# Kernel tuning notes

Hardware: AMD Instinct MI355X
Metric: run time of the kernel (lower is better)

## Reference

```python
import jax, jax.numpy as jnp
import numpy as np

B, N, D, NE, NB = 512, 128, 64, 6, 4

def setup_inputs() -> dict:
    key = jax.random.key(0)
    ks = jax.random.split(key, 24)
    inp = {}
    inp['atom_types'] = jax.random.randint(ks[0], (B, N), 0, NE, dtype=jnp.int32)
    inp['positions'] = jax.random.normal(ks[1], (B, N, 3), dtype=jnp.float32)
    inp['bonds'] = jax.random.randint(ks[2], (B, N, N), 0, 5, dtype=jnp.int32)
    s = 0.05
    inp['emb'] = jax.random.normal(ks[3], (NE, D), dtype=jnp.float32)
    inp['ae_w'] = jax.random.normal(ks[4], (D,), dtype=jnp.float32) * s
    inp['ae_b'] = jax.random.normal(ks[5], (), dtype=jnp.float32) * s
    inp['ent_w'] = jax.random.normal(ks[6], (D,), dtype=jnp.float32) * s
    inp['ent_b'] = jax.random.normal(ks[7], (), dtype=jnp.float32) * s
    inp['bW'] = jax.random.normal(ks[8], (NB, D, D), dtype=jnp.float32) * s
    inp['bb'] = jax.random.normal(ks[9], (NB,), dtype=jnp.float32) * s
    H = N * D
    inp['sW1'] = jax.random.normal(ks[10], (H, 256), dtype=jnp.float32) * s
    inp['sb1'] = jnp.zeros((256,), jnp.float32)
    inp['sW2'] = jax.random.normal(ks[11], (256, 128), dtype=jnp.float32) * s
    inp['sb2'] = jnp.zeros((128,), jnp.float32)
    inp['sW3'] = jax.random.normal(ks[12], (128, 1), dtype=jnp.float32) * s
    inp['sb3'] = jnp.zeros((1,), jnp.float32)
    inp['dW1'] = jax.random.normal(ks[13], (H, 256), dtype=jnp.float32) * s
    inp['db1'] = jnp.zeros((256,), jnp.float32)
    inp['dW2'] = jax.random.normal(ks[14], (256, 128), dtype=jnp.float32) * s
    inp['db2'] = jnp.zeros((128,), jnp.float32)
    inp['dW3'] = jax.random.normal(ks[15], (128, 1), dtype=jnp.float32) * s
    inp['db3'] = jnp.zeros((1,), jnp.float32)
    return inp

def _mlp(x, W1, b1, W2, b2, W3, b3):
    h = jax.nn.relu(x @ W1 + b1)
    h = jax.nn.relu(h @ W2 + b2)
    return jax.nn.sigmoid((h @ W3 + b3)[..., 0])

def reference(atom_types, positions, bonds, emb, ae_w, ae_b, ent_w, ent_b, bW, bb,
              sW1, sb1, sW2, sb2, sW3, sb3, dW1, db1, dW2, db2, dW3, db3):
    x = emb[atom_types]                                    # [B,N,D]
    atomic_e = jnp.einsum('bnd,d->bn', x, ae_w) + ae_b     # atomic_energy linear
    atomic_s = jnp.einsum('bnd,d->bn', x, ent_w) + ent_b   # atomic_entropy linear

    # Pairwise bilinear bond energies: e[b,i,j,k] = x_i^T W_k x_j + bb_k
    t = jnp.einsum('bid,kde->bike', x, bW)                 # [B,N,K,D]
    e_all = jnp.einsum('bike,bje->bijk', t, x) + bb        # [B,N,N,K]
    bt = bonds - 1                                         # bond type index
    upper = jnp.triu(jnp.ones((N, N), dtype=bool), k=1)    # i < j
    bond_mask = upper[None] & (bonds > 0) & (bt < NB)
    e_sel = jnp.take_along_axis(e_all, jnp.clip(bt, 0, NB - 1)[..., None].astype(jnp.int32), axis=-1)[..., 0]
    bond_e = jnp.sum(jnp.where(bond_mask, e_sel, 0.0), axis=(1, 2))

    # Lennard-Jones style vdW over all i<j pairs
    diff = positions[:, :, None, :] - positions[:, None, :, :]   # [B,N,N,3]
    dist = jnp.sqrt(jnp.sum(diff * diff, axis=-1))
    vmask = upper[None] & (dist > 0)
    inv = 1.0 / jnp.where(dist > 0, dist, 1.0)
    vdw = 4.0 * (inv ** 12 - inv ** 6) * 0.1
    vdw_e = jnp.sum(jnp.where(vmask, vdw, 0.0), axis=(1, 2))

    energy = atomic_e.sum(axis=1) + bond_e + vdw_e

    # entropy: unbiased variance over atoms, summed over xyz
    pos_var = jnp.var(positions, axis=1, ddof=1).sum(axis=-1)
    entropy = atomic_s.sum(axis=1) + jnp.log(1.0 + pos_var)

    mol = x.reshape(x.shape[0], -1)                        # [B, N*D]
    stability = _mlp(mol, sW1, sb1, sW2, sb2, sW3, sb3)
    druglikeness = _mlp(mol, dW1, db1, dW2, db2, dW3, db3)
    return (energy, entropy, stability, druglikeness, x)
```

## Files before the change

### kernel.cpp

```cpp
#include <hip/hip_runtime.h>
#include <math.h>

#define BB_ 512
#define NN_ 128
#define DD_ 64
#define NE_ 6
#define NB_ 4

#define WS_PAIRE 0
#define WS_E1    160
#define U16BASE_ 1024
#define TDOFF_   (768 * 256)
#define W2OFF_   (1536 * 256)

typedef unsigned short u16x8 __attribute__((ext_vector_type(8)));

__device__ __forceinline__ ushort f2b(float f) {
  unsigned u = __float_as_uint(f);
  u += 0x7FFFu + ((u >> 16) & 1u);
  return (ushort)(u >> 16);
}
__device__ __forceinline__ float b2f(ushort h) {
  return __uint_as_float(((unsigned)h) << 16);
}

__device__ __forceinline__ float block_reduce256(float v, volatile float* red4,
                                                 int tid) {
#pragma unroll
  for (int off = 32; off > 0; off >>= 1) v += __shfl_down(v, off);
  __syncthreads();
  if ((tid & 63) == 0) red4[tid >> 6] = v;
  __syncthreads();
  return red4[0] + red4[1] + red4[2] + red4[3];
}

__global__ __launch_bounds__(256, 4) void k_a(
    const float* __restrict__ emb, const float* __restrict__ ae_w,
    const float* __restrict__ ae_b, const float* __restrict__ ent_w,
    const float* __restrict__ ent_b, const float* __restrict__ bW,
    const float* __restrict__ sW1, const float* __restrict__ dW1,
    const float* __restrict__ sW2, const float* __restrict__ dW2,
    const int* __restrict__ atom_types, const float* __restrict__ pos,
    float* __restrict__ ws, float* __restrict__ out) {
  int id = blockIdx.x;
  int tid = threadIdx.x;
  ushort* U = (ushort*)(ws + U16BASE_);
  __shared__ float smem[1160];
  volatile float* red4 = smem + 1152;

  if (id < 1536) {
    int m = id / 3;
    int c = id - m * 3;
    if (c == 0) {
      int n = m >> 2;
      int which = (m >> 1) & 1;
      int ohalf = m & 1;
      const float* W1 = which ? dW1 : sW1;
      ushort* T = U + (which ? TDOFF_ : 0);
      float* e_s = smem;
      float* part = smem + 384;
      for (int i = tid; i < NE_ * DD_; i += 256) e_s[i] = emb[i];
      __syncthreads();
      int o_local = tid & 127;
      int dhalf = tid >> 7;
      int o = ohalf * 128 + o_local;
      float acc[NE_] = {0.f, 0.f, 0.f, 0.f, 0.f, 0.f};
      const float* Wp = W1 + ((size_t)(n * DD_ + dhalf * 32)) * 256 + o;
#pragma unroll 8
      for (int d = 0; d < 32; ++d) {
        float w = Wp[(size_t)d * 256];
#pragma unroll
        for (int t = 0; t < NE_; ++t)
          acc[t] += e_s[t * DD_ + dhalf * 32 + d] * w;
      }
      if (dhalf == 1) {
#pragma unroll
        for (int t = 0; t < NE_; ++t) part[t * 128 + o_local] = acc[t];
      }
      __syncthreads();
      if (dhalf == 0) {
#pragma unroll
        for (int t = 0; t < NE_; ++t)
          T[(n * NE_ + t) * 256 + o] = f2b(acc[t] + part[t * 128 + o_local]);
      }
    } else if (c == 1) {
      float* e_s = smem;
      unsigned char* tyb = (unsigned char*)(smem + 384);
      for (int i = tid; i < NE_ * DD_; i += 256) e_s[i] = emb[i];
      if (tid < 32) {
        int4 t4 = ((const int4*)(atom_types + (size_t)m * NN_))[tid];
        uchar4 u4;
        u4.x = (unsigned char)t4.x;
        u4.y = (unsigned char)t4.y;
        u4.z = (unsigned char)t4.z;
        u4.w = (unsigned char)t4.w;
        ((uchar4*)tyb)[tid] = u4;
      }
      __syncthreads();
      float4* out4 = (float4*)(out + 2048 + (size_t)m * (NN_ * DD_));
#pragma unroll
      for (int u = 0; u < 8; ++u) {
        int li = tid + (u << 8);
        int n = li >> 4;
        int d0 = (li & 15) << 2;
        out4[li] = *(const float4*)&e_s[tyb[n] * DD_ + d0];
      }
    } else {
      float4* p4 = (float4*)smem;
      float* aev = smem + 520;
      float* entv = smem + 528;
      float* redm = smem + 544;
      if (tid < 128) {
        const float* pm = pos + (size_t)m * NN_ * 3 + 3 * tid;
        p4[tid] = make_float4(pm[0], pm[1], pm[2], 0.f);
      } else if (tid < 224) {
        int v = (tid - 128) >> 3;
        int l8 = tid & 7;
        int t = v - (v >= 6 ? 6 : 0);
        const float* wv = (v >= 6) ? ent_w : ae_w;
        const float* er = emb + t * DD_ + l8 * 8;
        const float* wr = wv + l8 * 8;
        float s = 0.f;
#pragma unroll
        for (int u = 0; u < 8; ++u) s += er[u] * wr[u];
#pragma unroll
        for (int off = 4; off > 0; off >>= 1) s += __shfl_down(s, off, 8);
        if (l8 == 0) {
          if (v < 6)
            aev[v] = s + ae_b[0];
          else
            entv[v - 6] = s + ent_b[0];
        }
      }
      __syncthreads();

      int i = tid >> 1;
      int half = tid & 1;
      float4 pi = p4[i];
      float vp = 0.f;
#pragma unroll 8
      for (int u = 0; u < 64; ++u) {
        int j = (half << 6) + u;
        float4 pj = p4[j];
        float dx = pi.x - pj.x;
        float dy = pi.y - pj.y;
        float dz = pi.z - pj.z;
        float d2 = dx * dx + dy * dy + dz * dz;
        if (j > i && d2 > 0.f) {
          float rc = __builtin_amdgcn_rcpf(d2);
          float r6 = rc * rc * rc;
          vp += 0.4f * (r6 * r6 - r6);
        }
      }

      float x = 0.f, y = 0.f, z = 0.f, sq = 0.f, ae = 0.f, en = 0.f;
      if (tid < 128) {
        float4 p = p4[tid];
        x = p.x;
        y = p.y;
        z = p.z;
        sq = x * x + y * y + z * z;
        int t = atom_types[(size_t)m * NN_ + tid];
        ae = aev[t];
        en = entv[t];
      }
      float vals[7] = {vp, x, y, z, sq, ae, en};
#pragma unroll
      for (int v = 0; v < 7; ++v) {
#pragma unroll
        for (int off = 32; off > 0; off >>= 1)
          vals[v] += __shfl_down(vals[v], off);
      }
      int wv2 = tid >> 6, ln = tid & 63;
      if (ln == 0) {
#pragma unroll
        for (int v = 0; v < 7; ++v) redm[wv2 * 8 + v] = vals[v];
      }
      __syncthreads();
      if (tid == 0) {
        float S[7];
#pragma unroll
        for (int v = 0; v < 7; ++v)
          S[v] = redm[v] + redm[8 + v] + redm[16 + v] + redm[24 + v];
        float var = (S[4] - (S[1] * S[1] + S[2] * S[2] + S[3] * S[3]) *
                                (1.f / NN_)) *
                    (1.f / (NN_ - 1));
        ws[WS_E1 + m] = S[0] + S[5];
        out[BB_ + m] = S[6] + logf(1.f + var);
      }
    }
  } else if (id < 1680) {
    int e = id - 1536;
    int k = e / 36;
    int rem = e - k * 36;
    int ti = rem / 6, tj = rem - (rem / 6) * 6;
    int d = tid & 63;
    int qd = tid >> 6;
    const float* Wrow = bW + ((size_t)k * DD_ + d) * DD_ + qd * 16;
    const float* xj = emb + tj * DD_ + qd * 16;
    float a = 0.f;
#pragma unroll
    for (int u = 0; u < 16; ++u) a += Wrow[u] * xj[u];
    float c = emb[ti * DD_ + d] * a;
    c = block_reduce256(c, red4, tid);
    if (tid == 0) ws[WS_PAIRE + e] = c;
  } else {
    int base = (id - 1680) * 4096 + tid;
#pragma unroll
    for (int u = 0; u < 16; ++u) {
      int e = base + u * 256;
      int head = e >> 15;
      int idx = e & 32767;
      const float* src = head ? dW2 : sW2;
      U[W2OFF_ + e] = f2b(src[idx]);
    }
  }
}

__global__ __launch_bounds__(256, 4) void k_b(
    const int* __restrict__ atom_types, const int* __restrict__ bonds,
    const float* __restrict__ bb, const float* __restrict__ sb1,
    const float* __restrict__ sb2, const float* __restrict__ sW3,
    const float* __restrict__ sb3, const float* __restrict__ db1,
    const float* __restrict__ db2, const float* __restrict__ dW3,
    const float* __restrict__ db3, const float* __restrict__ ws,
    float* __restrict__ out) {
  int id = blockIdx.x;
  int tid = threadIdx.x;
  const ushort* U = (const ushort*)(ws + U16BASE_);
  __shared__ float smem[2632];
  volatile float* red4 = smem + 2624;

  if ((id & 1) == 0) {
    int m = id >> 1;
    float* pE = smem;
    float* bbv = smem + 144;
    unsigned char* tyb = (unsigned char*)(smem + 160);

    if (tid < 32) {
      int4 t4 = ((const int4*)(atom_types + (size_t)m * NN_))[tid];
      uchar4 u4;
      u4.x = (unsigned char)t4.x;
      u4.y = (unsigned char)t4.y;
      u4.z = (unsigned char)t4.z;
      u4.w = (unsigned char)t4.w;
      ((uchar4*)tyb)[tid] = u4;
    }
    if (tid >= 64 && tid < 208) pE[tid - 64] = ws[WS_PAIRE + tid - 64];
    if (tid >= 224 && tid < 228) bbv[tid - 224] = bb[tid - 224];
    __syncthreads();

    const int4* b4 = (const int4*)(bonds + (size_t)m * NN_ * NN_);
    float bp = 0.f;
#pragma unroll 4
    for (int it = 0; it < 16; ++it) {
      int li = tid + (it << 8);
      int i = li >> 5;
      int c = li & 31;
      if (c * 4 + 3 > i) {
        int4 v = b4[li];
        int j0 = c << 2;
        int ti6 = tyb[i] * 6;
        if (j0 + 0 > i && v.x > 0)
          bp += pE[(v.x - 1) * 36 + ti6 + tyb[j0 + 0]] + bbv[v.x - 1];
        if (j0 + 1 > i && v.y > 0)
          bp += pE[(v.y - 1) * 36 + ti6 + tyb[j0 + 1]] + bbv[v.y - 1];
        if (j0 + 2 > i && v.z > 0)
          bp += pE[(v.z - 1) * 36 + ti6 + tyb[j0 + 2]] + bbv[v.z - 1];
        if (j0 + 3 > i && v.w > 0)
          bp += pE[(v.w - 1) * 36 + ti6 + tyb[j0 + 3]] + bbv[v.w - 1];
      }
    }
    float e = block_reduce256(bp, red4, tid);
    if (tid == 0) out[m] = e + ws[WS_E1 + m];
  } else {
    int mlpid = id >> 1;
    int which = mlpid & 1;
    int mbase = (mlpid >> 1) * 2;
    float* part = smem;
    float* scr = smem;
    float* h2 = smem + 512;
    float* h1 = smem + 2048;
    unsigned char* tyb = (unsigned char*)(smem + 2560);

    tyb[tid] = (unsigned char)atom_types[(size_t)mbase * NN_ + tid];
    __syncthreads();

    {
      int mi = tid >> 7;
      int q = (tid >> 5) & 3;
      int ot = tid & 31;
      const ushort* Tb = U + (which ? TDOFF_ : 0) + ot * 8;
      const unsigned char* ty = tyb + mi * NN_;
      float a[8] = {0.f, 0.f, 0.f, 0.f, 0.f, 0.f, 0.f, 0.f};
      int nb = q * 32;
      for (int n0 = 0; n0 < 32; n0 += 8) {
        u16x8 v[8];
#pragma unroll
        for (int u = 0; u < 8; ++u) {
          int n = nb + n0 + u;
          v[u] = *(const u16x8*)(Tb + ((n * 6 + (int)ty[n]) << 8));
        }
#pragma unroll
        for (int u = 0; u < 8; ++u) {
#pragma unroll
          for (int j = 0; j < 8; ++j) a[j] += b2f(v[u][j]);
        }
      }
      float* pp = part + mi * 1024 + q * 256 + ot * 8;
#pragma unroll
      for (int j = 0; j < 8; ++j) pp[j] = a[j];
    }
    __syncthreads();
    {
#pragma unroll
      for (int li = tid; li < 512; li += 256) {
        int mm = li >> 8;
        int o = li & 255;
        float s = part[mm * 1024 + o] + part[mm * 1024 + 256 + o] +
                  part[mm * 1024 + 512 + o] + part[mm * 1024 + 768 + o];
        h1[li] = fmaxf(s + (which ? db1 : sb1)[o], 0.f);
      }
    }
    __syncthreads();

    {
      int k = tid & 127;
      int kh = tid >> 7;
      const ushort* Wp = U + W2OFF_ + which * 32768 + kh * 16384 + k;
      float acc[2] = {0.f, 0.f};
      for (int o0 = 0; o0 < 128; o0 += 16) {
        float wf[16];
#pragma unroll
        for (int u = 0; u < 16; ++u) wf[u] = b2f(Wp[(o0 + u) << 7]);
#pragma unroll
        for (int mm = 0; mm < 2; ++mm) {
          const float* hp = h1 + mm * 256 + kh * 128 + o0;
          float s = 0.f;
#pragma unroll
          for (int u = 0; u < 16; ++u) s += hp[u] * wf[u];
          acc[mm] += s;
        }
      }
      scr[kh * 256 + 0 * 128 + k] = acc[0];
      scr[kh * 256 + 1 * 128 + k] = acc[1];
    }
    __syncthreads();
    if (tid < 128) {
      float b2v = (which ? db2 : sb2)[tid];
#pragma unroll
      for (int mm = 0; mm < 2; ++mm)
        h2[mm * 128 + tid] =
            fmaxf(b2v + scr[mm * 128 + tid] + scr[256 + mm * 128 + tid], 0.f);
    }
    __syncthreads();

    {
      int mm = tid >> 5;
      int ln = tid & 31;
      if (mm < 2) {
        const float* W3 = which ? dW3 : sW3;
        float s = 0.f;
#pragma unroll
        for (int u = 0; u < 4; ++u) {
          int kk = ln + (u << 5);
          s += h2[mm * 128 + kk] * W3[kk];
        }
#pragma unroll
        for (int off = 16; off > 0; off >>= 1) s += __shfl_down(s, off, 32);
        if (ln == 0) {
          float b3 = (which ? db3 : sb3)[0];
          out[(2 + which) * BB_ + mbase + mm] = 1.f / (1.f + __expf(-(s + b3)));
        }
      }
    }
  }
}

extern "C" void kernel_launch(void* const* d_in, const int* in_sizes, int n_in,
                              void* d_out, int out_size, void* d_ws,
                              size_t ws_size, hipStream_t stream) {
  const int* atom_types = (const int*)d_in[0];
  const float* positions = (const float*)d_in[1];
  const int* bonds = (const int*)d_in[2];
  const float* emb = (const float*)d_in[3];
  const float* ae_w = (const float*)d_in[4];
  const float* ae_b = (const float*)d_in[5];
  const float* ent_w = (const float*)d_in[6];
  const float* ent_b = (const float*)d_in[7];
  const float* bW = (const float*)d_in[8];
  const float* bb = (const float*)d_in[9];
  const float* sW1 = (const float*)d_in[10];
  const float* sb1 = (const float*)d_in[11];
  const float* sW2 = (const float*)d_in[12];
  const float* sb2 = (const float*)d_in[13];
  const float* sW3 = (const float*)d_in[14];
  const float* sb3 = (const float*)d_in[15];
  const float* dW1 = (const float*)d_in[16];
  const float* db1 = (const float*)d_in[17];
  const float* dW2 = (const float*)d_in[18];
  const float* db2 = (const float*)d_in[19];
  const float* dW3 = (const float*)d_in[20];
  const float* db3 = (const float*)d_in[21];
  float* out = (float*)d_out;
  float* ws = (float*)d_ws;

  hipLaunchKernelGGL(k_a, dim3(1696), dim3(256), 0, stream, emb, ae_w, ae_b,
                     ent_w, ent_b, bW, sW1, dW1, sW2, dW2, atom_types,
                     positions, ws, out);
  hipLaunchKernelGGL(k_b, dim3(1024), dim3(256), 0, stream, atom_types, bonds,
                     bb, sb1, sb2, sW3, sb3, db1, db2, dW3, db3, ws, out);
}
```

Baseline: 28.08 us.

## Move independent per-molecule work from first kernel into second kernel

The vdW/entropy reduction and the embedding gather into the output do not depend on the precomputed tables, so they move from k_a into k_b. k_b now runs four block roles per molecule (2048 blocks), while k_a shrinks to the table-building work plus one block that zeroes the energy output. Energy is combined with atomicAdd from the bond and vdW blocks. The aim is a shorter dependency-bound first kernel and better-filled second launch, at the cost of atomics and a larger, more heterogeneous k_b.

```diff
diff --git a/kernel.cpp b/kernel.cpp
--- a/kernel.cpp
+++ b/kernel.cpp
@@ -8,7 +8,6 @@
 #define NB_ 4
 
 #define WS_PAIRE 0
-#define WS_E1    160
 #define U16BASE_ 1024
 #define TDOFF_   (768 * 256)
 #define W2OFF_   (1536 * 256)
@@ -35,162 +34,47 @@
 }
 
 __global__ __launch_bounds__(256, 4) void k_a(
-    const float* __restrict__ emb, const float* __restrict__ ae_w,
-    const float* __restrict__ ae_b, const float* __restrict__ ent_w,
-    const float* __restrict__ ent_b, const float* __restrict__ bW,
+    const float* __restrict__ emb, const float* __restrict__ bW,
     const float* __restrict__ sW1, const float* __restrict__ dW1,
     const float* __restrict__ sW2, const float* __restrict__ dW2,
-    const int* __restrict__ atom_types, const float* __restrict__ pos,
     float* __restrict__ ws, float* __restrict__ out) {
-  int id = blockIdx.x;
+  int blk = blockIdx.x;
   int tid = threadIdx.x;
   ushort* U = (ushort*)(ws + U16BASE_);
-  __shared__ float smem[1160];
-  volatile float* red4 = smem + 1152;
-
-  if (id < 1536) {
-    int m = id / 3;
-    int c = id - m * 3;
-    if (c == 0) {
-      int n = m >> 2;
-      int which = (m >> 1) & 1;
-      int ohalf = m & 1;
-      const float* W1 = which ? dW1 : sW1;
-      ushort* T = U + (which ? TDOFF_ : 0);
-      float* e_s = smem;
-      float* part = smem + 384;
-      for (int i = tid; i < NE_ * DD_; i += 256) e_s[i] = emb[i];
-      __syncthreads();
-      int o_local = tid & 127;
-      int dhalf = tid >> 7;
-      int o = ohalf * 128 + o_local;
-      float acc[NE_] = {0.f, 0.f, 0.f, 0.f, 0.f, 0.f};
-      const float* Wp = W1 + ((size_t)(n * DD_ + dhalf * 32)) * 256 + o;
+
+  if (blk < 512) {
+    int n = blk >> 2;
+    int which = (blk >> 1) & 1;
+    int ohalf = blk & 1;
+    const float* W1 = which ? dW1 : sW1;
+    ushort* T = U + (which ? TDOFF_ : 0);
+    __shared__ float e_s[NE_ * DD_];
+    __shared__ float part[NE_][128];
+    for (int i = tid; i < NE_ * DD_; i += 256) e_s[i] = emb[i];
+    __syncthreads();
+    int o_local = tid & 127;
+    int dhalf = tid >> 7;
+    int o = ohalf * 128 + o_local;
+    float acc[NE_] = {0.f, 0.f, 0.f, 0.f, 0.f, 0.f};
+    const float* Wp = W1 + ((size_t)(n * DD_ + dhalf * 32)) * 256 + o;
 #pragma unroll 8
-      for (int d = 0; d < 32; ++d) {
-        float w = Wp[(size_t)d * 256];
-#pragma unroll
-        for (int t = 0; t < NE_; ++t)
-          acc[t] += e_s[t * DD_ + dhalf * 32 + d] * w;
-      }
-      if (dhalf == 1) {
-#pragma unroll
-        for (int t = 0; t < NE_; ++t) part[t * 128 + o_local] = acc[t];
-      }
-      __syncthreads();
-      if (dhalf == 0) {
-#pragma unroll
-        for (int t = 0; t < NE_; ++t)
-          T[(n * NE_ + t) * 256 + o] = f2b(acc[t] + part[t * 128 + o_local]);
-      }
-    } else if (c == 1) {
-      float* e_s = smem;
-      unsigned char* tyb = (unsigned char*)(smem + 384);
-      for (int i = tid; i < NE_ * DD_; i += 256) e_s[i] = emb[i];
-      if (tid < 32) {
-        int4 t4 = ((const int4*)(atom_types + (size_t)m * NN_))[tid];
-        uchar4 u4;
-        u4.x = (unsigned char)t4.x;
-        u4.y = (unsigned char)t4.y;
-        u4.z = (unsigned char)t4.z;
-        u4.w = (unsigned char)t4.w;
-        ((uchar4*)tyb)[tid] = u4;
-      }
-      __syncthreads();
-      float4* out4 = (float4*)(out + 2048 + (size_t)m * (NN_ * DD_));
-#pragma unroll
-      for (int u = 0; u < 8; ++u) {
-        int li = tid + (u << 8);
-        int n = li >> 4;
-        int d0 = (li & 15) << 2;
-        out4[li] = *(const float4*)&e_s[tyb[n] * DD_ + d0];
-      }
-    } else {
-      float4* p4 = (float4*)smem;
-      float* aev = smem + 520;
-      float* entv = smem + 528;
-      float* redm = smem + 544;
-      if (tid < 128) {
-        const float* pm = pos + (size_t)m * NN_ * 3 + 3 * tid;
-        p4[tid] = make_float4(pm[0], pm[1], pm[2], 0.f);
-      } else if (tid < 224) {
-        int v = (tid - 128) >> 3;
-        int l8 = tid & 7;
-        int t = v - (v >= 6 ? 6 : 0);
-        const float* wv = (v >= 6) ? ent_w : ae_w;
-        const float* er = emb + t * DD_ + l8 * 8;
-        const float* wr = wv + l8 * 8;
-        float s = 0.f;
-#pragma unroll
-        for (int u = 0; u < 8; ++u) s += er[u] * wr[u];
-#pragma unroll
-        for (int off = 4; off > 0; off >>= 1) s += __shfl_down(s, off, 8);
-        if (l8 == 0) {
-          if (v < 6)
-            aev[v] = s + ae_b[0];
-          else
-            entv[v - 6] = s + ent_b[0];
-        }
-      }
-      __syncthreads();
-
-      int i = tid >> 1;
-      int half = tid & 1;
-      float4 pi = p4[i];
-      float vp = 0.f;
-#pragma unroll 8
-      for (int u = 0; u < 64; ++u) {
-        int j = (half << 6) + u;
-        float4 pj = p4[j];
-        float dx = pi.x - pj.x;
-        float dy = pi.y - pj.y;
-        float dz = pi.z - pj.z;
-        float d2 = dx * dx + dy * dy + dz * dz;
-        if (j > i && d2 > 0.f) {
-          float rc = __builtin_amdgcn_rcpf(d2);
-          float r6 = rc * rc * rc;
-          vp += 0.4f * (r6 * r6 - r6);
-        }
-      }
-
-      float x = 0.f, y = 0.f, z = 0.f, sq = 0.f, ae = 0.f, en = 0.f;
-      if (tid < 128) {
-        float4 p = p4[tid];
-        x = p.x;
-        y = p.y;
-        z = p.z;
-        sq = x * x + y * y + z * z;
-        int t = atom_types[(size_t)m * NN_ + tid];
-        ae = aev[t];
-        en = entv[t];
-      }
-      float vals[7] = {vp, x, y, z, sq, ae, en};
-#pragma unroll
-      for (int v = 0; v < 7; ++v) {
-#pragma unroll
-        for (int off = 32; off > 0; off >>= 1)
-          vals[v] += __shfl_down(vals[v], off);
-      }
-      int wv2 = tid >> 6, ln = tid & 63;
-      if (ln == 0) {
-#pragma unroll
-        for (int v = 0; v < 7; ++v) redm[wv2 * 8 + v] = vals[v];
-      }
-      __syncthreads();
-      if (tid == 0) {
-        float S[7];
-#pragma unroll
-        for (int v = 0; v < 7; ++v)
-          S[v] = redm[v] + redm[8 + v] + redm[16 + v] + redm[24 + v];
-        float var = (S[4] - (S[1] * S[1] + S[2] * S[2] + S[3] * S[3]) *
-                                (1.f / NN_)) *
-                    (1.f / (NN_ - 1));
-        ws[WS_E1 + m] = S[0] + S[5];
-        out[BB_ + m] = S[6] + logf(1.f + var);
-      }
-    }
-  } else if (id < 1680) {
-    int e = id - 1536;
+    for (int d = 0; d < 32; ++d) {
+      float w = Wp[(size_t)d * 256];
+#pragma unroll
+      for (int t = 0; t < NE_; ++t) acc[t] += e_s[t * DD_ + dhalf * 32 + d] * w;
+    }
+    if (dhalf == 1) {
+#pragma unroll
+      for (int t = 0; t < NE_; ++t) part[t][o_local] = acc[t];
+    }
+    __syncthreads();
+    if (dhalf == 0) {
+#pragma unroll
+      for (int t = 0; t < NE_; ++t)
+        T[(n * NE_ + t) * 256 + o] = f2b(acc[t] + part[t][o_local]);
+    }
+  } else if (blk < 656) {
+    int e = blk - 512;
     int k = e / 36;
     int rem = e - k * 36;
     int ti = rem / 6, tj = rem - (rem / 6) * 6;
@@ -202,10 +86,11 @@
 #pragma unroll
     for (int u = 0; u < 16; ++u) a += Wrow[u] * xj[u];
     float c = emb[ti * DD_ + d] * a;
+    __shared__ float red4[4];
     c = block_reduce256(c, red4, tid);
     if (tid == 0) ws[WS_PAIRE + e] = c;
-  } else {
-    int base = (id - 1680) * 4096 + tid;
+  } else if (blk < 672) {
+    int base = (blk - 656) * 4096 + tid;
 #pragma unroll
     for (int u = 0; u < 16; ++u) {
       int e = base + u * 256;
@@ -214,11 +99,16 @@
       const float* src = head ? dW2 : sW2;
       U[W2OFF_ + e] = f2b(src[idx]);
     }
+  } else {
+    ((float2*)out)[tid] = make_float2(0.f, 0.f);
   }
 }
 
 __global__ __launch_bounds__(256, 4) void k_b(
-    const int* __restrict__ atom_types, const int* __restrict__ bonds,
+    const int* __restrict__ atom_types, const float* __restrict__ pos,
+    const int* __restrict__ bonds, const float* __restrict__ emb,
+    const float* __restrict__ ae_w, const float* __restrict__ ae_b,
+    const float* __restrict__ ent_w, const float* __restrict__ ent_b,
     const float* __restrict__ bb, const float* __restrict__ sb1,
     const float* __restrict__ sb2, const float* __restrict__ sW3,
     const float* __restrict__ sb3, const float* __restrict__ db1,
@@ -226,13 +116,14 @@
     const float* __restrict__ db3, const float* __restrict__ ws,
     float* __restrict__ out) {
   int id = blockIdx.x;
+  int c = id & 3;
+  int m = id >> 2;
   int tid = threadIdx.x;
   const ushort* U = (const ushort*)(ws + U16BASE_);
-  __shared__ float smem[2632];
-  volatile float* red4 = smem + 2624;
-
-  if ((id & 1) == 0) {
-    int m = id >> 1;
+  __shared__ float smem[2640];
+  volatile float* red4 = smem + 2632;
+
+  if (c == 0) {
     float* pE = smem;
     float* bbv = smem + 144;
     unsigned char* tyb = (unsigned char*)(smem + 160);
@@ -256,10 +147,10 @@
     for (int it = 0; it < 16; ++it) {
       int li = tid + (it << 8);
       int i = li >> 5;
-      int c = li & 31;
-      if (c * 4 + 3 > i) {
+      int cc = li & 31;
+      if (cc * 4 + 3 > i) {
         int4 v = b4[li];
-        int j0 = c << 2;
+        int j0 = cc << 2;
         int ti6 = tyb[i] * 6;
         if (j0 + 0 > i && v.x > 0)
           bp += pE[(v.x - 1) * 36 + ti6 + tyb[j0 + 0]] + bbv[v.x - 1];
@@ -272,9 +163,114 @@
       }
     }
     float e = block_reduce256(bp, red4, tid);
-    if (tid == 0) out[m] = e + ws[WS_E1 + m];
+    if (tid == 0) atomicAdd(&out[m], e);
+  } else if (c == 1) {
+    float4* p4 = (float4*)smem;
+    float* aev = smem + 520;
+    float* entv = smem + 528;
+    float* redm = smem + 544;
+    if (tid < 128) {
+      const float* pm = pos + (size_t)m * NN_ * 3 + 3 * tid;
+      p4[tid] = make_float4(pm[0], pm[1], pm[2], 0.f);
+    } else if (tid < 224) {
+      int v = (tid - 128) >> 3;
+      int l8 = tid & 7;
+      int t = v - (v >= 6 ? 6 : 0);
+      const float* wv = (v >= 6) ? ent_w : ae_w;
+      const float* er = emb + t * DD_ + l8 * 8;
+      const float* wr = wv + l8 * 8;
+      float s = 0.f;
+#pragma unroll
+      for (int u = 0; u < 8; ++u) s += er[u] * wr[u];
+#pragma unroll
+      for (int off = 4; off > 0; off >>= 1) s += __shfl_down(s, off, 8);
+      if (l8 == 0) {
+        if (v < 6)
+          aev[v] = s + ae_b[0];
+        else
+          entv[v - 6] = s + ent_b[0];
+      }
+    }
+    __syncthreads();
+
+    int i = tid >> 1;
+    int half = tid & 1;
+    float4 pi = p4[i];
+    float vp = 0.f;
+#pragma unroll 8
+    for (int u = 0; u < 64; ++u) {
+      int j = (half << 6) + u;
+      float4 pj = p4[j];
+      float dx = pi.x - pj.x;
+      float dy = pi.y - pj.y;
+      float dz = pi.z - pj.z;
+      float d2 = dx * dx + dy * dy + dz * dz;
+      if (j > i && d2 > 0.f) {
+        float rc = __builtin_amdgcn_rcpf(d2);
+        float r6 = rc * rc * rc;
+        vp += 0.4f * (r6 * r6 - r6);
+      }
+    }
+
+    float x = 0.f, y = 0.f, z = 0.f, sq = 0.f, ae = 0.f, en = 0.f;
+    if (tid < 128) {
+      float4 p = p4[tid];
+      x = p.x;
+      y = p.y;
+      z = p.z;
+      sq = x * x + y * y + z * z;
+      int t = atom_types[(size_t)m * NN_ + tid];
+      ae = aev[t];
+      en = entv[t];
+    }
+    float vals[7] = {vp, x, y, z, sq, ae, en};
+#pragma unroll
+    for (int v = 0; v < 7; ++v) {
+#pragma unroll
+      for (int off = 32; off > 0; off >>= 1)
+        vals[v] += __shfl_down(vals[v], off);
+    }
+    int wv2 = tid >> 6, ln = tid & 63;
+    if (ln == 0) {
+#pragma unroll
+      for (int v = 0; v < 7; ++v) redm[wv2 * 8 + v] = vals[v];
+    }
+    __syncthreads();
+    if (tid == 0) {
+      float S[7];
+#pragma unroll
+      for (int v = 0; v < 7; ++v)
+        S[v] = redm[v] + redm[8 + v] + redm[16 + v] + redm[24 + v];
+      float var =
+          (S[4] - (S[1] * S[1] + S[2] * S[2] + S[3] * S[3]) * (1.f / NN_)) *
+          (1.f / (NN_ - 1));
+      atomicAdd(&out[m], S[0] + S[5]);
+      out[BB_ + m] = S[6] + logf(1.f + var);
+    }
+  } else if (c == 2) {
+    float* e_s = smem;
+    unsigned char* tyb = (unsigned char*)(smem + 384);
+    for (int i = tid; i < NE_ * DD_; i += 256) e_s[i] = emb[i];
+    if (tid < 32) {
+      int4 t4 = ((const int4*)(atom_types + (size_t)m * NN_))[tid];
+      uchar4 u4;
+      u4.x = (unsigned char)t4.x;
+      u4.y = (unsigned char)t4.y;
+      u4.z = (unsigned char)t4.z;
+      u4.w = (unsigned char)t4.w;
+      ((uchar4*)tyb)[tid] = u4;
+    }
+    __syncthreads();
+    float4* out4 = (float4*)(out + 2048 + (size_t)m * (NN_ * DD_));
+#pragma unroll
+    for (int u = 0; u < 8; ++u) {
+      int li = tid + (u << 8);
+      int n = li >> 4;
+      int d0 = (li & 15) << 2;
+      out4[li] = *(const float4*)&e_s[tyb[n] * DD_ + d0];
+    }
   } else {
-    int mlpid = id >> 1;
+    int mlpid = id >> 2;
     int which = mlpid & 1;
     int mbase = (mlpid >> 1) * 2;
     float* part = smem;
@@ -405,9 +401,9 @@
   float* out = (float*)d_out;
   float* ws = (float*)d_ws;
 
-  hipLaunchKernelGGL(k_a, dim3(1696), dim3(256), 0, stream, emb, ae_w, ae_b,
-                     ent_w, ent_b, bW, sW1, dW1, sW2, dW2, atom_types,
-                     positions, ws, out);
-  hipLaunchKernelGGL(k_b, dim3(1024), dim3(256), 0, stream, atom_types, bonds,
-                     bb, sb1, sb2, sW3, sb3, db1, db2, dW3, db3, ws, out);
-}
+  hipLaunchKernelGGL(k_a, dim3(673), dim3(256), 0, stream, emb, bW, sW1, dW1,
+                     sW2, dW2, ws, out);
+  hipLaunchKernelGGL(k_b, dim3(2048), dim3(256), 0, stream, atom_types,
+                     positions, bonds, emb, ae_w, ae_b, ent_w, ent_b, bb, sb1,
+                     sb2, sW3, sb3, db1, db2, dW3, db3, ws, out);
+}
```

Result: slower. 33.59 us (+19.6%).
